# Kernel optimization log

Measured on AMD Instinct MI355X. Metric: run time of the kernel, lower is better.

The kernel has to match this reference:

```python
import jax, jax.numpy as jnp
import numpy as np

# KroneLinear dims (in_a must equal in_b per the source's matmul contraction)
IN_A = 128
IN_B = 128
OUT_A = 128
OUT_B = 128
N = 4096  # batch


def setup_inputs() -> dict:
    key = jax.random.key(0)
    k1, k2, k3, k4 = jax.random.split(key, 4)
    x = jax.random.normal(k1, (N, IN_A * IN_B), dtype=jnp.float32)
    weight_a = jax.random.normal(k2, (OUT_A, IN_A), dtype=jnp.float32) * 0.05
    weight_b = jax.random.normal(k3, (OUT_B, IN_B), dtype=jnp.float32) * 0.05
    bias = jax.random.normal(k4, (OUT_A * OUT_B,), dtype=jnp.float32) * 0.05
    return {"x": x, "weight_a": weight_a, "weight_b": weight_b, "bias": bias}


def reference(x, weight_a, weight_b, bias):
    # vx: view [-1, in_b, in_a] then permute(0,2,1) -> [N, in_a, in_b]
    vx = x.reshape(-1, IN_B, IN_A).transpose(0, 2, 1)
    # torch.matmul(weight_b, vx): contracts weight_b's in_b with vx's dim-1 (in_a)
    # -> [N, out_b, in_b]
    bvx = jnp.einsum('ok,nkj->noj', weight_b, vx)
    # bvx @ weight_a.T -> [N, out_b, out_a]
    bvxa = jnp.einsum('noj,aj->noa', bvx, weight_a)
    # permute(0,2,1) -> [N, out_a, out_b], flatten, add bias
    y = bvxa.transpose(0, 2, 1).reshape(-1, OUT_A * OUT_B) + bias
    return y
```

## Files before the change

kernel.cpp:

```cpp
#include <hip/hip_runtime.h>

typedef __bf16 bf16x8 __attribute__((ext_vector_type(8)));
typedef float f32x4 __attribute__((ext_vector_type(4)));
typedef unsigned int u32x4 __attribute__((ext_vector_type(4)));
typedef unsigned short u16x4 __attribute__((ext_vector_type(4)));

__device__ __forceinline__ unsigned short f2b(float f) {
  union { float f; unsigned int u; } a; a.f = f;
  unsigned int u = a.u;
  u += 0x7fffu + ((u >> 16) & 1u);
  return (unsigned short)(u >> 16);
}

#define LDW 136

__global__ void prep_weights(const float* __restrict__ wa,
                             const float* __restrict__ wb,
                             unsigned short* __restrict__ owa,
                             unsigned short* __restrict__ owb) {
  int t = blockIdx.x * 256 + threadIdx.x;
  if (t < 128 * 128) owa[t] = f2b(wa[t]);
  else               owb[t - 128 * 128] = f2b(wb[t - 128 * 128]);
}

__global__ __launch_bounds__(512, 8)
void krone_kernel(const float* __restrict__ x,
                  const unsigned short* __restrict__ wa,
                  const unsigned short* __restrict__ wb,
                  const float* __restrict__ bias,
                  float* __restrict__ out) {
  __shared__ unsigned short Mlds[128 * LDW];

  const int tid  = threadIdx.x;
  const int lane = tid & 63;
  const int w    = tid >> 6;
  const int quad = lane >> 4;
  const int l16  = lane & 15;

  const float* xrow = x + (size_t)blockIdx.x * 16384;
  #pragma unroll
  for (int i = 0; i < 8; ++i) {
    int idx = (i << 9) + tid;
    f32x4 v = *(const f32x4*)(xrow + (idx << 2));
    int r = idx >> 5;
    int c = (idx & 31) << 2;
    u16x4 h;
    h[0] = f2b(v[0]); h[1] = f2b(v[1]); h[2] = f2b(v[2]); h[3] = f2b(v[3]);
    *(u16x4*)&Mlds[r * LDW + c] = h;
  }

  bf16x8 wbf[4];
  {
    const unsigned short* wbr = wb + (w * 16 + l16) * 128 + quad * 8;
    #pragma unroll
    for (int kk = 0; kk < 4; ++kk)
      wbf[kk] = __builtin_bit_cast(bf16x8, *(const u32x4*)(wbr + kk * 32));
  }

  __syncthreads();

  u16x4 ur[8];
  #pragma unroll
  for (int m = 0; m < 8; ++m) {
    f32x4 acc = {0.f, 0.f, 0.f, 0.f};
    const unsigned short* mr = &Mlds[(m * 16 + l16) * LDW + quad * 8];
    #pragma unroll
    for (int kk = 0; kk < 4; ++kk) {
      u32x4 ua = *(const u32x4*)(mr + kk * 32);
      acc = __builtin_amdgcn_mfma_f32_16x16x32_bf16(
              __builtin_bit_cast(bf16x8, ua), wbf[kk], acc, 0, 0, 0);
    }
    u16x4 h;
    h[0] = f2b(acc[0]); h[1] = f2b(acc[1]); h[2] = f2b(acc[2]); h[3] = f2b(acc[3]);
    ur[m] = h;
  }

  __syncthreads();

  #pragma unroll
  for (int m = 0; m < 8; ++m)
    *(u16x4*)&Mlds[(w * 16 + l16) * LDW + m * 16 + quad * 4] = ur[m];

  float* orow = out + (size_t)blockIdx.x * 16384;
  #pragma unroll
  for (int m = 0; m < 8; ++m) {
    f32x4 acc = {0.f, 0.f, 0.f, 0.f};
    const unsigned short* war = wa + (m * 16 + l16) * 128 + quad * 8;
    const unsigned short* utr = &Mlds[(w * 16 + l16) * LDW + quad * 8];
    #pragma unroll
    for (int kk = 0; kk < 4; ++kk) {
      u32x4 ua = *(const u32x4*)(war + kk * 32);
      u32x4 ub = *(const u32x4*)(utr + kk * 32);
      acc = __builtin_amdgcn_mfma_f32_16x16x32_bf16(
              __builtin_bit_cast(bf16x8, ua),
              __builtin_bit_cast(bf16x8, ub), acc, 0, 0, 0);
    }
    int row0 = m * 16 + quad * 4;
    int col  = w * 16 + l16;
    #pragma unroll
    for (int i = 0; i < 4; ++i) {
      int r = row0 + i;
      orow[r * 128 + col] = acc[i] + bias[r * 128 + col];
    }
  }
}

extern "C" void kernel_launch(void* const* d_in, const int* in_sizes, int n_in,
                              void* d_out, int out_size, void* d_ws, size_t ws_size,
                              hipStream_t stream) {
  const float* x  = (const float*)d_in[0];
  const float* wa = (const float*)d_in[1];
  const float* wb = (const float*)d_in[2];
  const float* bs = (const float*)d_in[3];
  float* out = (float*)d_out;

  unsigned short* wsa = (unsigned short*)d_ws;
  unsigned short* wsb = wsa + 128 * 128;

  int N = in_sizes[0] / 16384;

  prep_weights<<<128, 256, 0, stream>>>(wa, wb, wsa, wsb);
  krone_kernel<<<N, 512, 0, stream>>>(x, wsa, wsb, bs, out);
}
```

Baseline: 534.9 us.

## Swap MFMA operands for vectorized output stores and pre-swizzle weight_a fragments

Stage 2 now uses the intermediate tile as the A operand, held in registers, and weight_a as the B operand. This makes each lane own 4 consecutive output columns, so the bias load and output store become 16-byte vector accesses instead of scalar strided ones. The prep kernel rewrites weight_a into per-lane MFMA fragment order, so global reads of it are fully contiguous per wave. The occupancy hint drops from 8 to 4 waves per SIMD, which lets the compiler use more registers at the cost of fewer resident blocks.

```diff
diff --git a/kernel.cpp b/kernel.cpp
--- a/kernel.cpp
+++ b/kernel.cpp
@@ -19,13 +19,22 @@
                              unsigned short* __restrict__ owa,
                              unsigned short* __restrict__ owb) {
   int t = blockIdx.x * 256 + threadIdx.x;
-  if (t < 128 * 128) owa[t] = f2b(wa[t]);
-  else               owb[t - 128 * 128] = f2b(wb[t - 128 * 128]);
+  if (t < 16384) {
+    int j    = t & 7;
+    int lane = (t >> 3) & 63;
+    int kk   = (t >> 9) & 3;
+    int mp   = t >> 11;
+    int quad = lane >> 4, l16 = lane & 15;
+    owa[t] = f2b(wa[(mp * 16 + l16) * 128 + kk * 32 + quad * 8 + j]);
+  } else {
+    int u = t - 16384;
+    owb[u] = f2b(wb[u]);
+  }
 }
 
-__global__ __launch_bounds__(512, 8)
+__global__ __launch_bounds__(512, 4)
 void krone_kernel(const float* __restrict__ x,
-                  const unsigned short* __restrict__ wa,
+                  const unsigned short* __restrict__ waf,
                   const unsigned short* __restrict__ wb,
                   const float* __restrict__ bias,
                   float* __restrict__ out) {
@@ -81,27 +90,30 @@
   for (int m = 0; m < 8; ++m)
     *(u16x4*)&Mlds[(w * 16 + l16) * LDW + m * 16 + quad * 4] = ur[m];
 
-  float* orow = out + (size_t)blockIdx.x * 16384;
-  #pragma unroll
-  for (int m = 0; m < 8; ++m) {
-    f32x4 acc = {0.f, 0.f, 0.f, 0.f};
-    const unsigned short* war = wa + (m * 16 + l16) * 128 + quad * 8;
+  bf16x8 uf[4];
+  {
     const unsigned short* utr = &Mlds[(w * 16 + l16) * LDW + quad * 8];
     #pragma unroll
+    for (int kk = 0; kk < 4; ++kk)
+      uf[kk] = __builtin_bit_cast(bf16x8, *(const u32x4*)(utr + kk * 32));
+  }
+
+  float* orow = out + (size_t)blockIdx.x * 16384;
+  const unsigned short* wafl = waf + lane * 8;
+  #pragma unroll
+  for (int mp = 0; mp < 8; ++mp) {
+    f32x4 acc = {0.f, 0.f, 0.f, 0.f};
+    #pragma unroll
     for (int kk = 0; kk < 4; ++kk) {
-      u32x4 ua = *(const u32x4*)(war + kk * 32);
-      u32x4 ub = *(const u32x4*)(utr + kk * 32);
+      u32x4 ub = *(const u32x4*)(wafl + (mp * 4 + kk) * 512);
       acc = __builtin_amdgcn_mfma_f32_16x16x32_bf16(
-              __builtin_bit_cast(bf16x8, ua),
-              __builtin_bit_cast(bf16x8, ub), acc, 0, 0, 0);
+              uf[kk], __builtin_bit_cast(bf16x8, ub), acc, 0, 0, 0);
     }
-    int row0 = m * 16 + quad * 4;
-    int col  = w * 16 + l16;
-    #pragma unroll
-    for (int i = 0; i < 4; ++i) {
-      int r = row0 + i;
-      orow[r * 128 + col] = acc[i] + bias[r * 128 + col];
-    }
+    int r  = mp * 16 + l16;
+    int c0 = w * 16 + quad * 4;
+    f32x4 b = *(const f32x4*)(bias + r * 128 + c0);
+    f32x4 y = acc + b;
+    *(f32x4*)(orow + r * 128 + c0) = y;
   }
 }
 
```

After: 475.5 us. 1.12x faster.
